# Optimization experiments

Measured on AMD Instinct MI355X. Metric: run time of the kernel, lower is better.

## Reference

```python
import jax, jax.numpy as jnp
import numpy as np

FEAT = 252 * 3  # 756, flattened feature dim


def setup_inputs() -> dict:
    key = jax.random.key(0)
    k1, k2, k3, k4 = jax.random.split(key, 4)
    B, T = 8, 2048
    Q, K, D = 8, 1024, 256  # num_quantizers, codebook_size, embedding_dim
    inputs = jax.random.normal(k1, (B, T, 252, 3), dtype=jnp.float32)
    codebooks = jax.random.normal(k2, (Q, K, D), dtype=jnp.float32) * 0.05
    w_in = jax.random.normal(k3, (FEAT, D), dtype=jnp.float32) * (1.0 / np.sqrt(FEAT))
    w_out = jax.random.normal(k4, (D, FEAT), dtype=jnp.float32) * (1.0 / np.sqrt(D))
    return {"inputs": inputs, "codebooks": codebooks, "w_in": w_in, "w_out": w_out}


def _residual_vq(z, codebooks):
    # z: [B, T, D]; codebooks: [Q, K, D]
    def step(carry, cb):
        residual, quant_sum = carry
        # squared L2 distances: [B, T, K]
        d = (jnp.sum(residual * residual, axis=-1, keepdims=True)
             - 2.0 * jnp.einsum("btd,kd->btk", residual, cb)
             + jnp.sum(cb * cb, axis=-1))
        idx = jnp.argmin(d, axis=-1)          # [B, T]
        q = cb[idx]                            # gather -> [B, T, D]
        return (residual - q, quant_sum + q), (q, idx)

    init = (z, jnp.zeros_like(z))
    (_, quant_sum), (all_q, all_idx) = jax.lax.scan(step, init, codebooks)
    return quant_sum, all_q, all_idx  # [B,T,D], [Q,B,T,D], [Q,B,T]


def reference(inputs, codebooks, w_in, w_out):
    B = inputs.shape[0]
    # (B, T, 252, 3) -> (B, T, 3, 252) -> (B, T, 756)
    x = jnp.transpose(inputs, (0, 1, 3, 2)).reshape(B, -1, FEAT)
    z = jnp.einsum("btf,fd->btd", x, w_in)
    quant_sum, all_q, all_idx = _residual_vq(z, codebooks)
    quantized = jnp.einsum("btd,df->btf", quant_sum, w_out)
    quantized = jax.nn.relu(quantized)
    encoding_indices = jnp.transpose(all_idx, (1, 2, 0))  # [B, T, Q]
    return quantized, all_q, encoding_indices
```

## Files before the change

kernel.cpp:

```cpp
#include <hip/hip_runtime.h>
#include <float.h>

#define M_TOK 16384
#define DIM   256
#define NCODE 1024
#define NQ    8
#define FEAT  756
#define DSCALE 0.00375f
#define LCAP  2560
#define L2CAP 512

using short8 = __attribute__((ext_vector_type(8))) short;
using f32x4  = __attribute__((ext_vector_type(4))) float;

__device__ __forceinline__ float fm(float a, float b) { return __fmul_rn(a, b); }
__device__ __forceinline__ float fa(float a, float b) { return __fadd_rn(a, b); }
__device__ __forceinline__ float fs(float a, float b) { return __fsub_rn(a, b); }

__device__ __forceinline__ unsigned fkey(float f) {
  unsigned b = __float_as_uint(f);
  return (b & 0x80000000u) ? ~b : (b | 0x80000000u);
}
__device__ __forceinline__ float funkey(unsigned k) {
  unsigned b = (k & 0x80000000u) ? (k & 0x7FFFFFFFu) : ~k;
  return __uint_as_float(b);
}
__device__ __forceinline__ unsigned short bf16rne(float x) {
  unsigned b = __float_as_uint(x);
  return (unsigned short)((b + 0x7FFFu + ((b >> 16) & 1u)) >> 16);
}

__device__ __forceinline__ void gload_lds16(const void* g, void* l) {
  __builtin_amdgcn_global_load_lds(
      (const __attribute__((address_space(1))) unsigned int*)g,
      (__attribute__((address_space(3))) unsigned int*)l, 16, 0, 0);
}

__device__ float pairwise128_sq(const float* a) {
  float V[8][4];
#pragma unroll
  for (int j = 0; j < 8; ++j)
#pragma unroll
    for (int l = 0; l < 4; ++l) { float x = a[4 * j + l]; V[j][l] = fm(x, x); }
#pragma unroll
  for (int t = 1; t < 4; ++t)
#pragma unroll
    for (int j = 0; j < 8; ++j)
#pragma unroll
      for (int l = 0; l < 4; ++l) {
        float x = a[32 * t + 4 * j + l];
        V[j][l] = fa(V[j][l], fm(x, x));
      }
  float W[4];
#pragma unroll
  for (int l = 0; l < 4; ++l) {
    float p01 = fa(V[0][l], V[1][l]), p23 = fa(V[2][l], V[3][l]);
    float p45 = fa(V[4][l], V[5][l]), p67 = fa(V[6][l], V[7][l]);
    W[l] = fa(fa(p01, p23), fa(p45, p67));
  }
  return fa(fa(W[0], W[2]), fa(W[1], W[3]));
}
__device__ float pairwise256_sq(const float* a) {
  return fa(pairwise128_sq(a), pairwise128_sq(a + 128));
}

__device__ float dot256_np(const float* __restrict__ r, const float* __restrict__ c) {
  float L0 = 0.f, L1 = 0.f, L2 = 0.f, L3 = 0.f;
#pragma unroll 8
  for (int t = 0; t < 64; ++t) {
    float4 rv = *reinterpret_cast<const float4*>(r + 4 * t);
    float4 cv = *reinterpret_cast<const float4*>(c + 4 * t);
    L0 = fa(L0, fm(rv.x, cv.x));
    L1 = fa(L1, fm(rv.y, cv.y));
    L2 = fa(L2, fm(rv.z, cv.z));
    L3 = fa(L3, fm(rv.w, cv.w));
  }
  return fa(fa(L0, L2), fa(L1, L3));
}

__global__ __launch_bounds__(256) void k_z(const float* __restrict__ in,
                                           const float* __restrict__ w_in,
                                           float* __restrict__ residual) {
  const int m0 = blockIdx.x * 16;
  __shared__ __align__(16) float xp[16][FEAT];
  __shared__ __align__(16) float wsb[2][12][256];
  for (int i = threadIdx.x; i < 16 * FEAT; i += 256) {
    int t = i / FEAT, F = i - t * FEAT;
    int f = F / 3, c = F - f * 3;
    xp[t][c * 252 + f] = in[(size_t)m0 * FEAT + i];
  }
  const int dg = threadIdx.x & 63;
  const int tg = threadIdx.x >> 6;
#pragma unroll
  for (int k = 0; k < 3; ++k) {
    int fi = threadIdx.x + k * 256, row = fi >> 6, col = (fi & 63) * 4;
    *reinterpret_cast<float4*>(&wsb[0][row][col]) =
        *reinterpret_cast<const float4*>(&w_in[(size_t)row * DIM + col]);
  }
  __syncthreads();
  float4 a0 = {0.f, 0.f, 0.f, 0.f}, a1 = {0.f, 0.f, 0.f, 0.f};
  float4 a2 = {0.f, 0.f, 0.f, 0.f}, a3 = {0.f, 0.f, 0.f, 0.f};
  const float* xr0 = &xp[tg * 4 + 0][0];
  const float* xr1 = &xp[tg * 4 + 1][0];
  const float* xr2 = &xp[tg * 4 + 2][0];
  const float* xr3 = &xp[tg * 4 + 3][0];
  int cur = 0;
  for (int ch = 0; ch < 63; ++ch) {
    float4 nx[3];
    const bool hn = (ch + 1 < 63);
    if (hn) {
#pragma unroll
      for (int k = 0; k < 3; ++k) {
        int fi = threadIdx.x + k * 256, row = fi >> 6, col = (fi & 63) * 4;
        nx[k] = *reinterpret_cast<const float4*>(
            &w_in[((size_t)(ch + 1) * 12 + row) * DIM + col]);
      }
    }
#pragma unroll
    for (int j4 = 0; j4 < 3; ++j4) {
      float4 x0v = *reinterpret_cast<const float4*>(&xr0[ch * 12 + j4 * 4]);
      float4 x1v = *reinterpret_cast<const float4*>(&xr1[ch * 12 + j4 * 4]);
      float4 x2v = *reinterpret_cast<const float4*>(&xr2[ch * 12 + j4 * 4]);
      float4 x3v = *reinterpret_cast<const float4*>(&xr3[ch * 12 + j4 * 4]);
      float xs0[4] = {x0v.x, x0v.y, x0v.z, x0v.w};
      float xs1[4] = {x1v.x, x1v.y, x1v.z, x1v.w};
      float xs2[4] = {x2v.x, x2v.y, x2v.z, x2v.w};
      float xs3[4] = {x3v.x, x3v.y, x3v.z, x3v.w};
#pragma unroll
      for (int jj = 0; jj < 4; ++jj) {
        float4 w4 = *reinterpret_cast<const float4*>(&wsb[cur][j4 * 4 + jj][dg * 4]);
        float x0 = xs0[jj], x1 = xs1[jj], x2 = xs2[jj], x3 = xs3[jj];
        a0.x = fa(a0.x, fm(x0, w4.x)); a0.y = fa(a0.y, fm(x0, w4.y));
        a0.z = fa(a0.z, fm(x0, w4.z)); a0.w = fa(a0.w, fm(x0, w4.w));
        a1.x = fa(a1.x, fm(x1, w4.x)); a1.y = fa(a1.y, fm(x1, w4.y));
        a1.z = fa(a1.z, fm(x1, w4.z)); a1.w = fa(a1.w, fm(x1, w4.w));
        a2.x = fa(a2.x, fm(x2, w4.x)); a2.y = fa(a2.y, fm(x2, w4.y));
        a2.z = fa(a2.z, fm(x2, w4.z)); a2.w = fa(a2.w, fm(x2, w4.w));
        a3.x = fa(a3.x, fm(x3, w4.x)); a3.y = fa(a3.y, fm(x3, w4.y));
        a3.z = fa(a3.z, fm(x3, w4.z)); a3.w = fa(a3.w, fm(x3, w4.w));
      }
    }
    if (hn) {
#pragma unroll
      for (int k = 0; k < 3; ++k) {
        int fi = threadIdx.x + k * 256, row = fi >> 6, col = (fi & 63) * 4;
        *reinterpret_cast<float4*>(&wsb[cur ^ 1][row][col]) = nx[k];
      }
    }
    __syncthreads();
    cur ^= 1;
  }
  *reinterpret_cast<float4*>(&residual[(size_t)(m0 + tg * 4 + 0) * DIM + dg * 4]) = a0;
  *reinterpret_cast<float4*>(&residual[(size_t)(m0 + tg * 4 + 1) * DIM + dg * 4]) = a1;
  *reinterpret_cast<float4*>(&residual[(size_t)(m0 + tg * 4 + 2) * DIM + dg * 4]) = a2;
  *reinterpret_cast<float4*>(&residual[(size_t)(m0 + tg * 4 + 3) * DIM + dg * 4]) = a3;
}

__global__ __launch_bounds__(256) void k_cbnorm(const float* __restrict__ cb,
                                                float* __restrict__ cbn) {
  int row = blockIdx.x * 256 + threadIdx.x;
  if (row >= NQ * NCODE) return;
  cbn[row] = pairwise256_sq(&cb[(size_t)row * DIM]);
}

__global__ __launch_bounds__(256) void k_cb16(const float* __restrict__ cb,
                                              unsigned short* __restrict__ cb16) {
  size_t i = (size_t)blockIdx.x * 1024 + (size_t)threadIdx.x * 4;
  float4 v = *reinterpret_cast<const float4*>(&cb[i]);
  ushort4 o;
  o.x = bf16rne(v.x); o.y = bf16rne(v.y); o.z = bf16rne(v.z); o.w = bf16rne(v.w);
  *reinterpret_cast<ushort4*>(&cb16[i]) = o;
}

__global__ __launch_bounds__(256) void k_wt(const float* __restrict__ w_out,
                                            unsigned short* __restrict__ wT16) {
  int n = blockIdx.x, k = threadIdx.x;
  float v = (n < FEAT) ? w_out[(size_t)k * FEAT + n] : 0.f;
  wT16[(size_t)n * DIM + k] = bf16rne(v);
}

__global__ __launch_bounds__(256) void k_t1(const float* __restrict__ residual,
                                            float* __restrict__ t1g,
                                            unsigned long long* __restrict__ best64) {
  int m = blockIdx.x * 256 + threadIdx.x;
  t1g[m] = pairwise256_sq(&residual[(size_t)m * DIM]);
  best64[m] = 0xFFFFFFFFFFFFFFFFull;
}

__global__ __launch_bounds__(512) void k_screen(
    const unsigned short* __restrict__ cb16, const float* __restrict__ cb,
    const float* __restrict__ cbn, float* __restrict__ residual,
    float* __restrict__ t1g, unsigned long long* __restrict__ best64,
    float* __restrict__ allq, float* __restrict__ idxout, int q) {
  __shared__ __align__(16) unsigned short BsLin[2 * 64 * 256];
  __shared__ float cbn_s[NCODE];
  __shared__ unsigned list[LCAP];
  __shared__ unsigned list2[L2CAP];
  __shared__ unsigned fbs_u[64];
  __shared__ float t1_s[64], dlt_s[64];
  __shared__ unsigned lcnt, l2cnt, ovf;
  const int m0 = blockIdx.x * 64;
  const int tid = threadIdx.x, w = tid >> 6, lane = tid & 63;
  const int lrow = lane & 15, lk = lane >> 4;
  const int wg = w & 3, grp = w >> 2;
  const unsigned short* cbq16 = cb16 + (size_t)q * NCODE * DIM;
  const float* cbqf = cb + (size_t)q * NCODE * DIM;

  for (int i = tid; i < NCODE; i += 512) cbn_s[i] = cbn[q * NCODE + i];
  if (tid < 64) {
    float t1 = t1g[m0 + tid];
    t1_s[tid] = t1;
    dlt_s[tid] = fmaxf(DSCALE * sqrtf(fmaxf(t1, 0.f)), 1e-5f);
    fbs_u[tid] = 0xFFFFFFFFu;
  }
  if (tid == 0) { lcnt = 0; l2cnt = 0; ovf = 0; }

  short8 afr[8];
  {
    const float* rrow = &residual[(size_t)(m0 + wg * 16 + lrow) * DIM];
#pragma unroll
    for (int s = 0; s < 8; ++s) {
      float4 x0 = *reinterpret_cast<const float4*>(&rrow[s * 32 + lk * 8]);
      float4 x1 = *reinterpret_cast<const float4*>(&rrow[s * 32 + lk * 8 + 4]);
      short8 t;
      t[0] = (short)bf16rne(x0.x); t[1] = (short)bf16rne(x0.y);
      t[2] = (short)bf16rne(x0.z); t[3] = (short)bf16rne(x0.w);
      t[4] = (short)bf16rne(x1.x); t[5] = (short)bf16rne(x1.y);
      t[6] = (short)bf16rne(x1.z); t[7] = (short)bf16rne(x1.w);
      afr[s] = t;
    }
  }

#define STAGE(CT, B)                                                             \
  {                                                                              \
    _Pragma("unroll")                                                            \
    for (int k_ = 0; k_ < 4; ++k_) {                                             \
      int c_ = (w * 4 + k_) * 64 + lane;                                         \
      int row_ = c_ >> 5, c16_ = c_ & 31;                                        \
      const unsigned short* g_ =                                                 \
          &cbq16[(size_t)((CT) * 64 + row_) * 256 + (size_t)((c16_ ^ (row_ & 7)) * 8)]; \
      unsigned short* l_ = &BsLin[(B) * 16384 + (w * 4 + k_) * 512];             \
      gload_lds16(g_, l_);                                                       \
    }                                                                            \
  }

  STAGE(0, 0);
  __syncthreads();

  const int tokbase = wg * 16 + lk * 4;
  float dl[4];
#pragma unroll
  for (int r = 0; r < 4; ++r) dl[r] = dlt_s[tokbase + r];
  float runmin[4] = {FLT_MAX, FLT_MAX, FLT_MAX, FLT_MAX};
  int runcode[4] = {0, 0, 0, 0};

#define PUSH(PD, PC, R)                                                          \
  {                                                                              \
    unsigned idx_ = atomicAdd(&lcnt, 1u);                                        \
    if (idx_ < LCAP)                                                             \
      list[idx_] = (fkey(PD) & 0xFFFF0000u) |                                    \
                   ((unsigned)(tokbase + (R)) << 10) | (unsigned)(PC);           \
    else                                                                         \
      ovf = 1u;                                                                  \
  }

  for (int ct = 0; ct < 16; ++ct) {
    const int b = ct & 1;
    if (ct + 1 < 16) STAGE(ct + 1, b ^ 1);

    f32x4 acc[2];
    acc[0] = (f32x4){0.f, 0.f, 0.f, 0.f};
    acc[1] = (f32x4){0.f, 0.f, 0.f, 0.f};
#pragma unroll
    for (int s = 0; s < 8; ++s) {
#pragma unroll
      for (int f2 = 0; f2 < 2; ++f2) {
        const int f = grp * 2 + f2;
        const int row = f * 16 + lrow;
        const int chunk = (s * 4 + lk) ^ (lrow & 7);
        short8 bfr = *reinterpret_cast<const short8*>(
            &BsLin[b * 16384 + (size_t)row * 256 + chunk * 8]);
        acc[f2] = __builtin_amdgcn_mfma_f32_16x16x32_bf16(afr[s], bfr, acc[f2], 0, 0, 0);
      }
    }

#pragma unroll
    for (int f2 = 0; f2 < 2; ++f2) {
      const int code = ct * 64 + (grp * 2 + f2) * 16 + lrow;
      const float t3 = cbn_s[code];
#pragma unroll
      for (int r = 0; r < 4; ++r) {
        const float d = t3 - 2.0f * acc[f2][r];
        if (d < runmin[r]) {
          if (runmin[r] <= d + dl[r]) PUSH(runmin[r], runcode[r], r);
          runmin[r] = d; runcode[r] = code;
        } else if (d <= runmin[r] + dl[r]) {
          PUSH(d, code, r);
        }
      }
    }
    __syncthreads();
  }

  float fb[4] = {runmin[0], runmin[1], runmin[2], runmin[3]};
#pragma unroll
  for (int off = 8; off >= 1; off >>= 1)
#pragma unroll
    for (int r = 0; r < 4; ++r)
      fb[r] = fminf(fb[r], __shfl_xor(fb[r], off, 64));
#pragma unroll
  for (int r = 0; r < 4; ++r)
    if (runmin[r] <= fb[r] + dl[r]) PUSH(runmin[r], runcode[r], r);
  if (lrow == 0)
#pragma unroll
    for (int r = 0; r < 4; ++r)
      atomicMin(&fbs_u[tokbase + r], fkey(fb[r]));
  __syncthreads();

  {
    unsigned n = lcnt; if (n > LCAP) n = LCAP;
    for (unsigned i = tid; i < n; i += 512) {
      unsigned e = list[i];
      unsigned tok = (e >> 10) & 63u;
      float df = funkey(e & 0xFFFF0000u);
      if (df <= funkey(fbs_u[tok]) + dlt_s[tok]) {
        unsigned j = atomicAdd(&l2cnt, 1u);
        if (j < L2CAP) list2[j] = e & 0xFFFFu;
        else ovf = 1u;
      }
    }
  }
  __syncthreads();

  {
    unsigned n2 = l2cnt; if (n2 > L2CAP) n2 = L2CAP;
    const int j4 = lane & 3, g = lane >> 2;
    for (unsigned i0 = (unsigned)w * 16u; i0 < n2; i0 += 128u) {
      unsigned ci = i0 + (unsigned)g;
      bool act = ci < n2;
      unsigned ent = act ? list2[ci] : 0u;
      unsigned tok = (ent >> 10) & 63u, code = ent & 1023u;
      const float* rr = &residual[(size_t)(m0 + tok) * DIM];
      const float* cc2 = &cbqf[(size_t)code * DIM];
      float L = 0.f;
#pragma unroll 8
      for (int t = 0; t < 64; ++t)
        L = fa(L, fm(rr[4 * t + j4], cc2[4 * t + j4]));
      float tmp = fa(L, __shfl_xor(L, 2, 64));
      float e4 = fa(tmp, __shfl_xor(tmp, 1, 64));
      if (act && j4 == 0) {
        float dn = fa(fs(t1_s[tok], fa(e4, e4)), cbn_s[code]);
        atomicMin(&best64[m0 + tok],
                  ((unsigned long long)fkey(dn) << 32) | code);
      }
    }
  }
  __syncthreads();

  if (ovf) {
    const int j4 = lane & 3, g = lane >> 2;
    for (int t = 0; t < 8; ++t) {
      const int tok = w * 8 + t;
      const float* rr = &residual[(size_t)(m0 + tok) * DIM];
      for (int c0 = 0; c0 < NCODE; c0 += 16) {
        int code = c0 + g;
        const float* cc2 = &cbqf[(size_t)code * DIM];
        float L = 0.f;
        for (int tt = 0; tt < 64; ++tt)
          L = fa(L, fm(rr[4 * tt + j4], cc2[4 * tt + j4]));
        float tmp = fa(L, __shfl_xor(L, 2, 64));
        float e4 = fa(tmp, __shfl_xor(tmp, 1, 64));
        if (j4 == 0) {
          float dn = fa(fs(t1_s[tok], fa(e4, e4)), cbn_s[code]);
          atomicMin(&best64[m0 + tok],
                    ((unsigned long long)fkey(dn) << 32) | (unsigned)code);
        }
      }
    }
    __syncthreads();
  }

  for (int t = 0; t < 8; ++t) {
    const int tok = w * 8 + t;
    const size_t m = (size_t)m0 + tok;
    const int ci = (int)(best64[m] & 0xFFFFFFFFull);
    const float4 cv = *reinterpret_cast<const float4*>(&cbqf[(size_t)ci * DIM + lane * 4]);
    const size_t base = m * DIM + lane * 4;
    float4 r = *reinterpret_cast<const float4*>(&residual[base]);
    r.x = fs(r.x, cv.x); r.y = fs(r.y, cv.y); r.z = fs(r.z, cv.z); r.w = fs(r.w, cv.w);
    *reinterpret_cast<float4*>(&residual[base]) = r;
    *reinterpret_cast<float4*>(&allq[((size_t)q * M_TOK + m) * DIM + lane * 4]) = cv;
    float qs[4] = {fm(r.x, r.x), fm(r.y, r.y), fm(r.z, r.z), fm(r.w, r.w)};
    float W[4];
#pragma unroll
    for (int l = 0; l < 4; ++l) {
      float v = qs[l];
      float s1 = __shfl_down(v, 8, 64);
      float s2 = __shfl_down(v, 16, 64);
      float s3 = __shfl_down(v, 24, 64);
      float V = fa(fa(fa(v, s1), s2), s3);
      float A = fa(V, __shfl_down(V, 1, 64));
      float B = fa(A, __shfl_down(A, 2, 64));
      W[l] = fa(B, __shfl_down(B, 4, 64));
    }
    float hsum = fa(fa(W[0], W[2]), fa(W[1], W[3]));
    float up = __shfl(hsum, 32, 64);
    if (lane == 0) {
      t1g[m] = fa(hsum, up);
      best64[m] = 0xFFFFFFFFFFFFFFFFull;
      idxout[m * NQ + q] = (float)ci;
    }
  }
#undef PUSH
#undef STAGE
}

__global__ __launch_bounds__(256) void k_gemm_out(const float* __restrict__ allq,
                                                  const unsigned short* __restrict__ wT16,
                                                  float* __restrict__ C) {
  __shared__ __align__(16) unsigned short As[64][264];
  __shared__ __align__(16) unsigned short Bs[64][264];
  const int m0 = blockIdx.x * 64;
  const int tid = threadIdx.x, w = tid >> 6, lane = tid & 63;
  const int lrow = lane & 15, lk = lane >> 4;

#pragma unroll
  for (int k4 = 0; k4 < 16; ++k4) {
    int f4 = tid + k4 * 256;
    int tok = f4 >> 6, dseg = f4 & 63;
    float4 v = {0.f, 0.f, 0.f, 0.f};
#pragma unroll
    for (int qq = 0; qq < NQ; ++qq) {
      float4 t = *reinterpret_cast<const float4*>(
          &allq[((size_t)qq * M_TOK + m0 + tok) * DIM + dseg * 4]);
      v.x = fa(v.x, t.x); v.y = fa(v.y, t.y); v.z = fa(v.z, t.z); v.w = fa(v.w, t.w);
    }
    ushort4 o;
    o.x = bf16rne(v.x); o.y = bf16rne(v.y); o.z = bf16rne(v.z); o.w = bf16rne(v.w);
    *reinterpret_cast<ushort4*>(&As[tok][dseg * 4]) = o;
  }
  __syncthreads();

  short8 afr[8];
#pragma unroll
  for (int s = 0; s < 8; ++s)
    afr[s] = *reinterpret_cast<const short8*>(&As[w * 16 + lrow][s * 32 + lk * 8]);

  for (int nt = 0; nt < 12; ++nt) {
    const int n0 = nt * 64;
    __syncthreads();
    {
      int r = tid >> 2, seg = tid & 3;
      const uint4* src = reinterpret_cast<const uint4*>(&wT16[(size_t)(n0 + r) * DIM + seg * 64]);
      uint4* dst = reinterpret_cast<uint4*>(&Bs[r][seg * 64]);
#pragma unroll
      for (int u = 0; u < 8; ++u) dst[u] = src[u];
    }
    __syncthreads();

    f32x4 acc[4];
#pragma unroll
    for (int f = 0; f < 4; ++f) acc[f] = (f32x4){0.f, 0.f, 0.f, 0.f};
#pragma unroll
    for (int s = 0; s < 8; ++s) {
#pragma unroll
      for (int f = 0; f < 4; ++f) {
        short8 bfr = *reinterpret_cast<const short8*>(&Bs[f * 16 + lrow][s * 32 + lk * 8]);
        acc[f] = __builtin_amdgcn_mfma_f32_16x16x32_bf16(afr[s], bfr, acc[f], 0, 0, 0);
      }
    }

#pragma unroll
    for (int f = 0; f < 4; ++f) {
      const int col = n0 + f * 16 + lrow;
      if (col < FEAT) {
#pragma unroll
        for (int r = 0; r < 4; ++r)
          C[(size_t)(m0 + w * 16 + lk * 4 + r) * FEAT + col] = fmaxf(acc[f][r], 0.f);
      }
    }
  }
}

extern "C" void kernel_launch(void* const* d_in, const int* in_sizes, int n_in,
                              void* d_out, int out_size, void* d_ws, size_t ws_size,
                              hipStream_t stream) {
  int i_inputs = 0, i_cb = 1, iA = 2, iB = 3;
  {
    int a = -1, b = -1, ii = -1, ic = -1;
    for (int i = 0; i < n_in; ++i) {
      if (in_sizes[i] == M_TOK * FEAT) ii = i;
      else if (in_sizes[i] == NQ * NCODE * DIM) ic = i;
      else if (in_sizes[i] == FEAT * DIM) { if (a < 0) a = i; else b = i; }
    }
    if (ii >= 0 && ic >= 0 && a >= 0 && b >= 0) { i_inputs = ii; i_cb = ic; iA = a; iB = b; }
  }
  const float* inputs = (const float*)d_in[i_inputs];
  const float* cb     = (const float*)d_in[i_cb];
  const float* w_in   = (const float*)d_in[iA];
  const float* w_out  = (const float*)d_in[iB];

  float* out       = (float*)d_out;
  float* quantized = out;
  float* allq      = out + (size_t)M_TOK * FEAT;
  float* idxout    = allq + (size_t)NQ * M_TOK * DIM;

  float* residual = quantized;

  char* ws = (char*)d_ws;
  unsigned short*     cb16   = (unsigned short*)(ws);
  unsigned short*     wT16   = (unsigned short*)(ws + 4194304);
  float*              cbn    = (float*)(ws + 4587520);
  float*              t1g    = (float*)(ws + 4620288);
  unsigned long long* best64 = (unsigned long long*)(ws + 4685824);

  k_z<<<M_TOK / 16, 256, 0, stream>>>(inputs, w_in, residual);
  k_cbnorm<<<NQ * NCODE / 256, 256, 0, stream>>>(cb, cbn);
  k_cb16<<<NQ * NCODE * DIM / 1024, 256, 0, stream>>>(cb, cb16);
  k_wt<<<768, 256, 0, stream>>>(w_out, wT16);
  k_t1<<<M_TOK / 256, 256, 0, stream>>>(residual, t1g, best64);
  for (int q = 0; q < NQ; ++q)
    k_screen<<<M_TOK / 64, 512, 0, stream>>>(cb16, cb, cbn, residual, t1g, best64,
                                             allq, idxout, q);
  k_gemm_out<<<M_TOK / 64, 256, 0, stream>>>(allq, wT16, quantized);
}
```

Baseline: 632.3 us.

## Fuse all eight quantizer stages into one kernel with residual kept in LDS

Replaces the per-quantizer k_screen launches and the k_t1 kernel with a single k_vq8 kernel. Each block loads its 64-token residual tile into shared memory once and loops over all 8 codebooks, keeping the residual, squared norms and best-index state in LDS. This removes 8 launches and the global round trips for residual, t1 and best64. The cost is about 66KB more LDS per block (res_s), which may lower occupancy, and there are no longer kernel boundaries between stages to give scheduling slack.

```diff
diff --git a/kernel.cpp b/kernel.cpp
--- a/kernel.cpp
+++ b/kernel.cpp
@@ -62,20 +62,6 @@
 }
 __device__ float pairwise256_sq(const float* a) {
   return fa(pairwise128_sq(a), pairwise128_sq(a + 128));
-}
-
-__device__ float dot256_np(const float* __restrict__ r, const float* __restrict__ c) {
-  float L0 = 0.f, L1 = 0.f, L2 = 0.f, L3 = 0.f;
-#pragma unroll 8
-  for (int t = 0; t < 64; ++t) {
-    float4 rv = *reinterpret_cast<const float4*>(r + 4 * t);
-    float4 cv = *reinterpret_cast<const float4*>(c + 4 * t);
-    L0 = fa(L0, fm(rv.x, cv.x));
-    L1 = fa(L1, fm(rv.y, cv.y));
-    L2 = fa(L2, fm(rv.z, cv.z));
-    L3 = fa(L3, fm(rv.w, cv.w));
-  }
-  return fa(fa(L0, L2), fa(L1, L3));
 }
 
 __global__ __launch_bounds__(256) void k_z(const float* __restrict__ in,
@@ -179,240 +165,246 @@
   wT16[(size_t)n * DIM + k] = bf16rne(v);
 }
 
-__global__ __launch_bounds__(256) void k_t1(const float* __restrict__ residual,
-                                            float* __restrict__ t1g,
-                                            unsigned long long* __restrict__ best64) {
-  int m = blockIdx.x * 256 + threadIdx.x;
-  t1g[m] = pairwise256_sq(&residual[(size_t)m * DIM]);
-  best64[m] = 0xFFFFFFFFFFFFFFFFull;
-}
-
-__global__ __launch_bounds__(512) void k_screen(
+__global__ __launch_bounds__(512) void k_vq8(
     const unsigned short* __restrict__ cb16, const float* __restrict__ cb,
-    const float* __restrict__ cbn, float* __restrict__ residual,
-    float* __restrict__ t1g, unsigned long long* __restrict__ best64,
-    float* __restrict__ allq, float* __restrict__ idxout, int q) {
+    const float* __restrict__ cbn, const float* __restrict__ residual,
+    float* __restrict__ allq, float* __restrict__ idxout) {
   __shared__ __align__(16) unsigned short BsLin[2 * 64 * 256];
+  __shared__ __align__(16) float res_s[64][260];
   __shared__ float cbn_s[NCODE];
   __shared__ unsigned list[LCAP];
   __shared__ unsigned list2[L2CAP];
   __shared__ unsigned fbs_u[64];
   __shared__ float t1_s[64], dlt_s[64];
+  __shared__ unsigned long long best64_s[64];
   __shared__ unsigned lcnt, l2cnt, ovf;
   const int m0 = blockIdx.x * 64;
   const int tid = threadIdx.x, w = tid >> 6, lane = tid & 63;
   const int lrow = lane & 15, lk = lane >> 4;
   const int wg = w & 3, grp = w >> 2;
-  const unsigned short* cbq16 = cb16 + (size_t)q * NCODE * DIM;
-  const float* cbqf = cb + (size_t)q * NCODE * DIM;
-
-  for (int i = tid; i < NCODE; i += 512) cbn_s[i] = cbn[q * NCODE + i];
+
+  for (int i = tid; i < 64 * 64; i += 512) {
+    int tok = i >> 6, c4 = i & 63;
+    float4 v = *reinterpret_cast<const float4*>(&residual[(size_t)(m0 + tok) * DIM + c4 * 4]);
+    *reinterpret_cast<float4*>(&res_s[tok][c4 * 4]) = v;
+  }
+  __syncthreads();
   if (tid < 64) {
-    float t1 = t1g[m0 + tid];
-    t1_s[tid] = t1;
-    dlt_s[tid] = fmaxf(DSCALE * sqrtf(fmaxf(t1, 0.f)), 1e-5f);
-    fbs_u[tid] = 0xFFFFFFFFu;
-  }
-  if (tid == 0) { lcnt = 0; l2cnt = 0; ovf = 0; }
-
-  short8 afr[8];
-  {
-    const float* rrow = &residual[(size_t)(m0 + wg * 16 + lrow) * DIM];
-#pragma unroll
-    for (int s = 0; s < 8; ++s) {
-      float4 x0 = *reinterpret_cast<const float4*>(&rrow[s * 32 + lk * 8]);
-      float4 x1 = *reinterpret_cast<const float4*>(&rrow[s * 32 + lk * 8 + 4]);
-      short8 t;
-      t[0] = (short)bf16rne(x0.x); t[1] = (short)bf16rne(x0.y);
-      t[2] = (short)bf16rne(x0.z); t[3] = (short)bf16rne(x0.w);
-      t[4] = (short)bf16rne(x1.x); t[5] = (short)bf16rne(x1.y);
-      t[6] = (short)bf16rne(x1.z); t[7] = (short)bf16rne(x1.w);
-      afr[s] = t;
-    }
-  }
+    t1_s[tid] = pairwise256_sq(&res_s[tid][0]);
+    best64_s[tid] = 0xFFFFFFFFFFFFFFFFull;
+  }
+  __syncthreads();
+
+  for (int q = 0; q < NQ; ++q) {
+    const unsigned short* cbq16 = cb16 + (size_t)q * NCODE * DIM;
+    const float* cbqf = cb + (size_t)q * NCODE * DIM;
+
+    for (int i = tid; i < NCODE; i += 512) cbn_s[i] = cbn[q * NCODE + i];
+    if (tid < 64) {
+      dlt_s[tid] = fmaxf(DSCALE * sqrtf(fmaxf(t1_s[tid], 0.f)), 1e-5f);
+      fbs_u[tid] = 0xFFFFFFFFu;
+    }
+    if (tid == 0) { lcnt = 0; l2cnt = 0; ovf = 0; }
+
+    short8 afr[8];
+    {
+      const float* rrow = &res_s[wg * 16 + lrow][0];
+#pragma unroll
+      for (int s = 0; s < 8; ++s) {
+        float4 x0 = *reinterpret_cast<const float4*>(&rrow[s * 32 + lk * 8]);
+        float4 x1 = *reinterpret_cast<const float4*>(&rrow[s * 32 + lk * 8 + 4]);
+        short8 t;
+        t[0] = (short)bf16rne(x0.x); t[1] = (short)bf16rne(x0.y);
+        t[2] = (short)bf16rne(x0.z); t[3] = (short)bf16rne(x0.w);
+        t[4] = (short)bf16rne(x1.x); t[5] = (short)bf16rne(x1.y);
+        t[6] = (short)bf16rne(x1.z); t[7] = (short)bf16rne(x1.w);
+        afr[s] = t;
+      }
+    }
 
 #define STAGE(CT, B)                                                             \
-  {                                                                              \
-    _Pragma("unroll")                                                            \
-    for (int k_ = 0; k_ < 4; ++k_) {                                             \
-      int c_ = (w * 4 + k_) * 64 + lane;                                         \
-      int row_ = c_ >> 5, c16_ = c_ & 31;                                        \
-      const unsigned short* g_ =                                                 \
-          &cbq16[(size_t)((CT) * 64 + row_) * 256 + (size_t)((c16_ ^ (row_ & 7)) * 8)]; \
-      unsigned short* l_ = &BsLin[(B) * 16384 + (w * 4 + k_) * 512];             \
-      gload_lds16(g_, l_);                                                       \
-    }                                                                            \
-  }
-
-  STAGE(0, 0);
-  __syncthreads();
-
-  const int tokbase = wg * 16 + lk * 4;
-  float dl[4];
-#pragma unroll
-  for (int r = 0; r < 4; ++r) dl[r] = dlt_s[tokbase + r];
-  float runmin[4] = {FLT_MAX, FLT_MAX, FLT_MAX, FLT_MAX};
-  int runcode[4] = {0, 0, 0, 0};
+    {                                                                            \
+      _Pragma("unroll")                                                          \
+      for (int k_ = 0; k_ < 4; ++k_) {                                           \
+        int c_ = (w * 4 + k_) * 64 + lane;                                       \
+        int row_ = c_ >> 5, c16_ = c_ & 31;                                      \
+        const unsigned short* g_ =                                               \
+            &cbq16[(size_t)((CT) * 64 + row_) * 256 + (size_t)((c16_ ^ (row_ & 7)) * 8)]; \
+        unsigned short* l_ = &BsLin[(B) * 16384 + (w * 4 + k_) * 512];           \
+        gload_lds16(g_, l_);                                                     \
+      }                                                                          \
+    }
+
+    STAGE(0, 0);
+    __syncthreads();
+
+    const int tokbase = wg * 16 + lk * 4;
+    float dl[4];
+#pragma unroll
+    for (int r = 0; r < 4; ++r) dl[r] = dlt_s[tokbase + r];
+    float runmin[4] = {FLT_MAX, FLT_MAX, FLT_MAX, FLT_MAX};
+    int runcode[4] = {0, 0, 0, 0};
 
 #define PUSH(PD, PC, R)                                                          \
-  {                                                                              \
-    unsigned idx_ = atomicAdd(&lcnt, 1u);                                        \
-    if (idx_ < LCAP)                                                             \
-      list[idx_] = (fkey(PD) & 0xFFFF0000u) |                                    \
-                   ((unsigned)(tokbase + (R)) << 10) | (unsigned)(PC);           \
-    else                                                                         \
-      ovf = 1u;                                                                  \
-  }
-
-  for (int ct = 0; ct < 16; ++ct) {
-    const int b = ct & 1;
-    if (ct + 1 < 16) STAGE(ct + 1, b ^ 1);
-
-    f32x4 acc[2];
-    acc[0] = (f32x4){0.f, 0.f, 0.f, 0.f};
-    acc[1] = (f32x4){0.f, 0.f, 0.f, 0.f};
-#pragma unroll
-    for (int s = 0; s < 8; ++s) {
+    {                                                                            \
+      unsigned idx_ = atomicAdd(&lcnt, 1u);                                      \
+      if (idx_ < LCAP)                                                           \
+        list[idx_] = (fkey(PD) & 0xFFFF0000u) |                                  \
+                     ((unsigned)(tokbase + (R)) << 10) | (unsigned)(PC);         \
+      else                                                                       \
+        ovf = 1u;                                                                \
+    }
+
+    for (int ct = 0; ct < 16; ++ct) {
+      const int b = ct & 1;
+      if (ct + 1 < 16) STAGE(ct + 1, b ^ 1);
+
+      f32x4 acc[2];
+      acc[0] = (f32x4){0.f, 0.f, 0.f, 0.f};
+      acc[1] = (f32x4){0.f, 0.f, 0.f, 0.f};
+#pragma unroll
+      for (int s = 0; s < 8; ++s) {
+#pragma unroll
+        for (int f2 = 0; f2 < 2; ++f2) {
+          const int f = grp * 2 + f2;
+          const int row = f * 16 + lrow;
+          const int chunk = (s * 4 + lk) ^ (lrow & 7);
+          short8 bfr = *reinterpret_cast<const short8*>(
+              &BsLin[b * 16384 + (size_t)row * 256 + chunk * 8]);
+          acc[f2] = __builtin_amdgcn_mfma_f32_16x16x32_bf16(afr[s], bfr, acc[f2], 0, 0, 0);
+        }
+      }
+
 #pragma unroll
       for (int f2 = 0; f2 < 2; ++f2) {
-        const int f = grp * 2 + f2;
-        const int row = f * 16 + lrow;
-        const int chunk = (s * 4 + lk) ^ (lrow & 7);
-        short8 bfr = *reinterpret_cast<const short8*>(
-            &BsLin[b * 16384 + (size_t)row * 256 + chunk * 8]);
-        acc[f2] = __builtin_amdgcn_mfma_f32_16x16x32_bf16(afr[s], bfr, acc[f2], 0, 0, 0);
-      }
-    }
-
-#pragma unroll
-    for (int f2 = 0; f2 < 2; ++f2) {
-      const int code = ct * 64 + (grp * 2 + f2) * 16 + lrow;
-      const float t3 = cbn_s[code];
-#pragma unroll
-      for (int r = 0; r < 4; ++r) {
-        const float d = t3 - 2.0f * acc[f2][r];
-        if (d < runmin[r]) {
-          if (runmin[r] <= d + dl[r]) PUSH(runmin[r], runcode[r], r);
-          runmin[r] = d; runcode[r] = code;
-        } else if (d <= runmin[r] + dl[r]) {
-          PUSH(d, code, r);
+        const int code = ct * 64 + (grp * 2 + f2) * 16 + lrow;
+        const float t3 = cbn_s[code];
+#pragma unroll
+        for (int r = 0; r < 4; ++r) {
+          const float d = t3 - 2.0f * acc[f2][r];
+          if (d < runmin[r]) {
+            if (runmin[r] <= d + dl[r]) PUSH(runmin[r], runcode[r], r);
+            runmin[r] = d; runcode[r] = code;
+          } else if (d <= runmin[r] + dl[r]) {
+            PUSH(d, code, r);
+          }
         }
       }
-    }
-    __syncthreads();
-  }
-
-  float fb[4] = {runmin[0], runmin[1], runmin[2], runmin[3]};
-#pragma unroll
-  for (int off = 8; off >= 1; off >>= 1)
+      __syncthreads();
+    }
+
+    float fb[4] = {runmin[0], runmin[1], runmin[2], runmin[3]};
+#pragma unroll
+    for (int off = 8; off >= 1; off >>= 1)
+#pragma unroll
+      for (int r = 0; r < 4; ++r)
+        fb[r] = fminf(fb[r], __shfl_xor(fb[r], off, 64));
 #pragma unroll
     for (int r = 0; r < 4; ++r)
-      fb[r] = fminf(fb[r], __shfl_xor(fb[r], off, 64));
-#pragma unroll
-  for (int r = 0; r < 4; ++r)
-    if (runmin[r] <= fb[r] + dl[r]) PUSH(runmin[r], runcode[r], r);
-  if (lrow == 0)
-#pragma unroll
-    for (int r = 0; r < 4; ++r)
-      atomicMin(&fbs_u[tokbase + r], fkey(fb[r]));
-  __syncthreads();
-
-  {
-    unsigned n = lcnt; if (n > LCAP) n = LCAP;
-    for (unsigned i = tid; i < n; i += 512) {
-      unsigned e = list[i];
-      unsigned tok = (e >> 10) & 63u;
-      float df = funkey(e & 0xFFFF0000u);
-      if (df <= funkey(fbs_u[tok]) + dlt_s[tok]) {
-        unsigned j = atomicAdd(&l2cnt, 1u);
-        if (j < L2CAP) list2[j] = e & 0xFFFFu;
-        else ovf = 1u;
-      }
-    }
-  }
-  __syncthreads();
-
-  {
-    unsigned n2 = l2cnt; if (n2 > L2CAP) n2 = L2CAP;
-    const int j4 = lane & 3, g = lane >> 2;
-    for (unsigned i0 = (unsigned)w * 16u; i0 < n2; i0 += 128u) {
-      unsigned ci = i0 + (unsigned)g;
-      bool act = ci < n2;
-      unsigned ent = act ? list2[ci] : 0u;
-      unsigned tok = (ent >> 10) & 63u, code = ent & 1023u;
-      const float* rr = &residual[(size_t)(m0 + tok) * DIM];
-      const float* cc2 = &cbqf[(size_t)code * DIM];
-      float L = 0.f;
+      if (runmin[r] <= fb[r] + dl[r]) PUSH(runmin[r], runcode[r], r);
+    if (lrow == 0)
+#pragma unroll
+      for (int r = 0; r < 4; ++r)
+        atomicMin(&fbs_u[tokbase + r], fkey(fb[r]));
+    __syncthreads();
+
+    {
+      unsigned n = lcnt; if (n > LCAP) n = LCAP;
+      for (unsigned i = tid; i < n; i += 512) {
+        unsigned e = list[i];
+        unsigned tok = (e >> 10) & 63u;
+        float df = funkey(e & 0xFFFF0000u);
+        if (df <= funkey(fbs_u[tok]) + dlt_s[tok]) {
+          unsigned j = atomicAdd(&l2cnt, 1u);
+          if (j < L2CAP) list2[j] = e & 0xFFFFu;
+          else ovf = 1u;
+        }
+      }
+    }
+    __syncthreads();
+
+    {
+      unsigned n2 = l2cnt; if (n2 > L2CAP) n2 = L2CAP;
+      const int j4 = lane & 3, g = lane >> 2;
+      for (unsigned i0 = (unsigned)w * 16u; i0 < n2; i0 += 128u) {
+        unsigned ci = i0 + (unsigned)g;
+        bool act = ci < n2;
+        unsigned ent = act ? list2[ci] : 0u;
+        unsigned tok = (ent >> 10) & 63u, code = ent & 1023u;
+        const float* rr = &res_s[tok][0];
+        const float* cc2 = &cbqf[(size_t)code * DIM];
+        float L = 0.f;
 #pragma unroll 8
-      for (int t = 0; t < 64; ++t)
-        L = fa(L, fm(rr[4 * t + j4], cc2[4 * t + j4]));
-      float tmp = fa(L, __shfl_xor(L, 2, 64));
-      float e4 = fa(tmp, __shfl_xor(tmp, 1, 64));
-      if (act && j4 == 0) {
-        float dn = fa(fs(t1_s[tok], fa(e4, e4)), cbn_s[code]);
-        atomicMin(&best64[m0 + tok],
-                  ((unsigned long long)fkey(dn) << 32) | code);
-      }
-    }
-  }
-  __syncthreads();
-
-  if (ovf) {
-    const int j4 = lane & 3, g = lane >> 2;
+        for (int t = 0; t < 64; ++t)
+          L = fa(L, fm(rr[4 * t + j4], cc2[4 * t + j4]));
+        float tmp = fa(L, __shfl_xor(L, 2, 64));
+        float e4 = fa(tmp, __shfl_xor(tmp, 1, 64));
+        if (act && j4 == 0) {
+          float dn = fa(fs(t1_s[tok], fa(e4, e4)), cbn_s[code]);
+          atomicMin(&best64_s[tok],
+                    ((unsigned long long)fkey(dn) << 32) | code);
+        }
+      }
+    }
+    __syncthreads();
+
+    if (ovf) {
+      const int j4 = lane & 3, g = lane >> 2;
+      for (int t = 0; t < 8; ++t) {
+        const int tok = w * 8 + t;
+        const float* rr = &res_s[tok][0];
+        for (int c0 = 0; c0 < NCODE; c0 += 16) {
+          int code = c0 + g;
+          const float* cc2 = &cbqf[(size_t)code * DIM];
+          float L = 0.f;
+          for (int tt = 0; tt < 64; ++tt)
+            L = fa(L, fm(rr[4 * tt + j4], cc2[4 * tt + j4]));
+          float tmp = fa(L, __shfl_xor(L, 2, 64));
+          float e4 = fa(tmp, __shfl_xor(tmp, 1, 64));
+          if (j4 == 0) {
+            float dn = fa(fs(t1_s[tok], fa(e4, e4)), cbn_s[code]);
+            atomicMin(&best64_s[tok],
+                      ((unsigned long long)fkey(dn) << 32) | (unsigned)code);
+          }
+        }
+      }
+      __syncthreads();
+    }
+
     for (int t = 0; t < 8; ++t) {
       const int tok = w * 8 + t;
-      const float* rr = &residual[(size_t)(m0 + tok) * DIM];
-      for (int c0 = 0; c0 < NCODE; c0 += 16) {
-        int code = c0 + g;
-        const float* cc2 = &cbqf[(size_t)code * DIM];
-        float L = 0.f;
-        for (int tt = 0; tt < 64; ++tt)
-          L = fa(L, fm(rr[4 * tt + j4], cc2[4 * tt + j4]));
-        float tmp = fa(L, __shfl_xor(L, 2, 64));
-        float e4 = fa(tmp, __shfl_xor(tmp, 1, 64));
-        if (j4 == 0) {
-          float dn = fa(fs(t1_s[tok], fa(e4, e4)), cbn_s[code]);
-          atomicMin(&best64[m0 + tok],
-                    ((unsigned long long)fkey(dn) << 32) | (unsigned)code);
-        }
-      }
-    }
-    __syncthreads();
-  }
-
-  for (int t = 0; t < 8; ++t) {
-    const int tok = w * 8 + t;
-    const size_t m = (size_t)m0 + tok;
-    const int ci = (int)(best64[m] & 0xFFFFFFFFull);
-    const float4 cv = *reinterpret_cast<const float4*>(&cbqf[(size_t)ci * DIM + lane * 4]);
-    const size_t base = m * DIM + lane * 4;
-    float4 r = *reinterpret_cast<const float4*>(&residual[base]);
-    r.x = fs(r.x, cv.x); r.y = fs(r.y, cv.y); r.z = fs(r.z, cv.z); r.w = fs(r.w, cv.w);
-    *reinterpret_cast<float4*>(&residual[base]) = r;
-    *reinterpret_cast<float4*>(&allq[((size_t)q * M_TOK + m) * DIM + lane * 4]) = cv;
-    float qs[4] = {fm(r.x, r.x), fm(r.y, r.y), fm(r.z, r.z), fm(r.w, r.w)};
-    float W[4];
-#pragma unroll
-    for (int l = 0; l < 4; ++l) {
-      float v = qs[l];
-      float s1 = __shfl_down(v, 8, 64);
-      float s2 = __shfl_down(v, 16, 64);
-      float s3 = __shfl_down(v, 24, 64);
-      float V = fa(fa(fa(v, s1), s2), s3);
-      float A = fa(V, __shfl_down(V, 1, 64));
-      float B = fa(A, __shfl_down(A, 2, 64));
-      W[l] = fa(B, __shfl_down(B, 4, 64));
-    }
-    float hsum = fa(fa(W[0], W[2]), fa(W[1], W[3]));
-    float up = __shfl(hsum, 32, 64);
-    if (lane == 0) {
-      t1g[m] = fa(hsum, up);
-      best64[m] = 0xFFFFFFFFFFFFFFFFull;
-      idxout[m * NQ + q] = (float)ci;
-    }
-  }
+      const size_t m = (size_t)m0 + tok;
+      const int ci = (int)(best64_s[tok] & 0xFFFFFFFFull);
+      const float4 cv = *reinterpret_cast<const float4*>(&cbqf[(size_t)ci * DIM + lane * 4]);
+      float4 r = *reinterpret_cast<const float4*>(&res_s[tok][lane * 4]);
+      r.x = fs(r.x, cv.x); r.y = fs(r.y, cv.y); r.z = fs(r.z, cv.z); r.w = fs(r.w, cv.w);
+      *reinterpret_cast<float4*>(&res_s[tok][lane * 4]) = r;
+      *reinterpret_cast<float4*>(&allq[((size_t)q * M_TOK + m) * DIM + lane * 4]) = cv;
+      float qs[4] = {fm(r.x, r.x), fm(r.y, r.y), fm(r.z, r.z), fm(r.w, r.w)};
+      float W[4];
+#pragma unroll
+      for (int l = 0; l < 4; ++l) {
+        float v = qs[l];
+        float s1 = __shfl_down(v, 8, 64);
+        float s2 = __shfl_down(v, 16, 64);
+        float s3 = __shfl_down(v, 24, 64);
+        float V = fa(fa(fa(v, s1), s2), s3);
+        float A = fa(V, __shfl_down(V, 1, 64));
+        float B = fa(A, __shfl_down(A, 2, 64));
+        W[l] = fa(B, __shfl_down(B, 4, 64));
+      }
+      float hsum = fa(fa(W[0], W[2]), fa(W[1], W[3]));
+      float up = __shfl(hsum, 32, 64);
+      if (lane == 0) {
+        t1_s[tok] = fa(hsum, up);
+        best64_s[tok] = 0xFFFFFFFFFFFFFFFFull;
+        idxout[m * NQ + q] = (float)ci;
+      }
+    }
+    __syncthreads();
 #undef PUSH
 #undef STAGE
+  }
 }
 
 __global__ __launch_bounds__(256) void k_gemm_out(const float* __restrict__ allq,
@@ -511,16 +503,11 @@
   unsigned short*     cb16   = (unsigned short*)(ws);
   unsigned short*     wT16   = (unsigned short*)(ws + 4194304);
   float*              cbn    = (float*)(ws + 4587520);
-  float*              t1g    = (float*)(ws + 4620288);
-  unsigned long long* best64 = (unsigned long long*)(ws + 4685824);
 
   k_z<<<M_TOK / 16, 256, 0, stream>>>(inputs, w_in, residual);
   k_cbnorm<<<NQ * NCODE / 256, 256, 0, stream>>>(cb, cbn);
   k_cb16<<<NQ * NCODE * DIM / 1024, 256, 0, stream>>>(cb, cb16);
   k_wt<<<768, 256, 0, stream>>>(w_out, wT16);
-  k_t1<<<M_TOK / 256, 256, 0, stream>>>(residual, t1g, best64);
-  for (int q = 0; q < NQ; ++q)
-    k_screen<<<M_TOK / 64, 512, 0, stream>>>(cb16, cb, cbn, residual, t1g, best64,
-                                             allq, idxout, q);
+  k_vq8<<<M_TOK / 64, 512, 0, stream>>>(cb16, cb, cbn, residual, allq, idxout);
   k_gemm_out<<<M_TOK / 64, 256, 0, stream>>>(allq, wT16, quantized);
 }
```

Result: faster. 535.1 us, median of 4 (-15.4%).
